# Kernel tuning notes

Hardware: AMD Instinct MI355X
Metric: run time of the kernel (lower is better)

Reference implementation:

```python
import jax, jax.numpy as jnp
import numpy as np

DIM = 256
N_CHANNELS = 8
NEIGHBORS = 16


def setup_inputs() -> dict:
    key = jax.random.key(0)
    kx, kw = jax.random.split(key)
    B, N, D = 4, 1024, DIM
    x = jax.random.normal(kx, (B, N, D), dtype=jnp.float32)
    # nn.Linear(dim, dim*2*n_channels, bias=False); store as [in, out] so y = x @ W
    W_qk = jax.random.normal(kw, (D, 2 * N_CHANNELS * D), dtype=jnp.float32) * (D ** -0.5)
    return {"x": x, "W_qk": W_qk}


def _norm_edge(edge):
    # edge: [B, C, N, N]
    norm_row = edge / (edge.sum(axis=-1, keepdims=True) + 1e-6)
    norm_col = norm_row / (norm_row.sum(axis=-2, keepdims=True) + 1e-6)
    # norm_row @ norm_col^T
    return jnp.einsum('bcnk,bcmk->bcnm', norm_row, norm_col)


def reference(x, W_qk):
    B, N, D = x.shape
    C = N_CHANNELS
    scale = D ** -0.5
    qk = (x @ W_qk).reshape(B, N, 2, C, D)
    q = jnp.transpose(qk[:, :, 0], (0, 2, 1, 3))  # [B, C, N, D]
    k = jnp.transpose(qk[:, :, 1], (0, 2, 1, 3))  # [B, C, N, D]
    attn = jax.nn.softmax(jnp.einsum('bcnd,bcmd->bcnm', q, k) * scale, axis=-1)

    # clip(): top-k neighbor mask from channel-summed (detached) attention
    sum_edge = jax.lax.stop_gradient(attn).sum(axis=1)  # [B, N, N]
    kk = min(NEIGHBORS, N)
    _, top_idx = jax.lax.top_k(sum_edge, kk)  # [B, N, kk]
    b_idx = jnp.arange(B)[:, None, None]
    r_idx = jnp.arange(N)[None, :, None]
    mask = jnp.zeros((B, N, N), dtype=attn.dtype).at[b_idx, r_idx, top_idx].set(1.0)
    mask = jnp.maximum(mask, jnp.eye(N, dtype=attn.dtype))  # identity diag
    edge = mask[:, None] * attn  # [B, C, N, N]
    return _norm_edge(edge)
```

## Files before the change

### kernel.cpp

```cpp
#include <hip/hip_runtime.h>
#include <hip/hip_bf16.h>
#include <math.h>

#define BB 4
#define NN 1024
#define DD 256
#define CC 8
#define KNBR 16
#define MAXSEL 17
#define ZCAP (NN * MAXSEL)

typedef _Float16 f16x8_t __attribute__((ext_vector_type(8)));
typedef _Float16 f16x4_t __attribute__((ext_vector_type(4)));
typedef float    f32x4_t __attribute__((ext_vector_type(4)));

__device__ __forceinline__ void gl2lds16(const _Float16* g, _Float16* ldsbase) {
    __builtin_amdgcn_global_load_lds(
        (const __attribute__((address_space(1))) unsigned int*)g,
        (__attribute__((address_space(3))) unsigned int*)ldsbase, 16, 0, 0);
}

__device__ __forceinline__ void split2(float v, _Float16& h, _Float16& l) {
    h = (_Float16)v;
    l = (_Float16)(v - (float)h);
}

__global__ __launch_bounds__(256) void split_all(const float* __restrict__ x,
                                                 const float* __restrict__ W,
                                                 _Float16* __restrict__ xh,
                                                 _Float16* __restrict__ xl,
                                                 _Float16* __restrict__ Wth,
                                                 _Float16* __restrict__ Wtl,
                                                 int* __restrict__ countb) {
    const int tid = threadIdx.x;
    if (blockIdx.x < 1024) {
        int i = (blockIdx.x * 256 + tid) * 4;
        float4 v = *(const float4*)(x + i);
        f16x4_t hv, lv;
        _Float16 h, l;
        split2(v.x, h, l); hv[0] = h; lv[0] = l;
        split2(v.y, h, l); hv[1] = h; lv[1] = l;
        split2(v.z, h, l); hv[2] = h; lv[2] = l;
        split2(v.w, h, l); hv[3] = h; lv[3] = l;
        *(f16x4_t*)(xh + i) = hv;
        *(f16x4_t*)(xl + i) = lv;
    } else {
        const int b2 = blockIdx.x - 1024;
        if (b2 == 0) {
            int4 zz = make_int4(0, 0, 0, 0);
#pragma unroll
            for (int g = 0; g < 4; g++) ((int4*)countb)[tid + 256 * g] = zz;
        }
        __shared__ float t[64][65];
        const int n0 = (b2 & 63) * 64;
        const int k0 = (b2 >> 6) * 64;
#pragma unroll
        for (int i = 0; i < 16; i++) {
            int k = i * 4 + (tid >> 6);
            int n = tid & 63;
            t[k][n] = W[(size_t)(k0 + k) * 4096 + n0 + n];
        }
        __syncthreads();
#pragma unroll
        for (int i = 0; i < 16; i++) {
            int n = i * 4 + (tid >> 6);
            int k = tid & 63;
            _Float16 h, l;
            split2(t[k][n] * 16.f, h, l);
            size_t o = (size_t)(n0 + n) * 256 + k0 + k;
            Wth[o] = h; Wtl[o] = l;
        }
    }
}

#define STG(dst, src, rowbase, kk)                                             \
    do {                                                                       \
        gl2lds16((src) + (size_t)((rowbase) + r_st) * 256 + (kk) + c8,         \
                 &(dst)[(w * 64) * 8]);                                        \
        gl2lds16((src) + (size_t)((rowbase) + 64 + r_st) * 256 + (kk) + c8,    \
                 &(dst)[(256 + w * 64) * 8]);                                  \
    } while (0)

#define MFMA3(accv, AH, AL, BH, BL)                                            \
    do {                                                                       \
        accv = __builtin_amdgcn_mfma_f32_16x16x32_f16(AL, BH, accv, 0, 0, 0);  \
        accv = __builtin_amdgcn_mfma_f32_16x16x32_f16(AH, BL, accv, 0, 0, 0);  \
        accv = __builtin_amdgcn_mfma_f32_16x16x32_f16(AH, BH, accv, 0, 0, 0);  \
    } while (0)

#define COMPUTE(AH, AL, BH, BL)                                                \
    do {                                                                       \
        f16x8_t ah[4], al[4];                                                  \
        _Pragma("unroll")                                                      \
        for (int mi = 0; mi < 4; mi++) {                                       \
            int r = (wr * 64 + mi * 16 + lm) * 32 + qx8;                       \
            ah[mi] = *(const f16x8_t*)&(AH)[r];                                \
            al[mi] = *(const f16x8_t*)&(AL)[r];                                \
        }                                                                      \
        _Pragma("unroll")                                                      \
        for (int ni = 0; ni < 4; ni++) {                                       \
            int rb = (wc * 64 + ni * 16 + lm) * 32 + qx8;                      \
            f16x8_t bh = *(const f16x8_t*)&(BH)[rb];                           \
            f16x8_t bl = *(const f16x8_t*)&(BL)[rb];                           \
            _Pragma("unroll")                                                  \
            for (int mi = 0; mi < 4; mi++)                                     \
                MFMA3(acc[mi][ni], ah[mi], al[mi], bh, bl);                    \
        }                                                                      \
    } while (0)

__global__ __launch_bounds__(256) void gemm_xw_mfma(
        const _Float16* __restrict__ xh, const _Float16* __restrict__ xl,
        const _Float16* __restrict__ wth, const _Float16* __restrict__ wtl,
        _Float16* __restrict__ qh, _Float16* __restrict__ ql,
        _Float16* __restrict__ kh, _Float16* __restrict__ kl) {
    __shared__ __align__(16) char smem[65536];
    _Float16* Ah0 = (_Float16*)smem;
    _Float16* Al0 = (_Float16*)(smem + 8192);
    _Float16* Bh0 = (_Float16*)(smem + 16384);
    _Float16* Bl0 = (_Float16*)(smem + 24576);
    _Float16* Ah1 = (_Float16*)(smem + 32768);
    _Float16* Al1 = (_Float16*)(smem + 40960);
    _Float16* Bh1 = (_Float16*)(smem + 49152);
    _Float16* Bl1 = (_Float16*)(smem + 57344);
    const int tid = threadIdx.x, lane = tid & 63, w = tid >> 6;
    const int wr = w >> 1, wc = w & 1;
    const int lm = lane & 15, quad = lane >> 4;
    const int row0 = blockIdx.y * 128, col0 = blockIdx.x * 128;
    const int r_st = tid >> 2;
    const int c8 = (((tid & 3) ^ ((tid >> 3) & 3)) * 8);
    const int qx8 = ((quad ^ ((lm >> 1) & 3)) * 8);

    f32x4_t acc[4][4];
#pragma unroll
    for (int i = 0; i < 4; i++)
#pragma unroll
        for (int j = 0; j < 4; j++) acc[i][j] = (f32x4_t)(0.f);

    STG(Ah0, xh, row0, 0); STG(Al0, xl, row0, 0);
    STG(Bh0, wth, col0, 0); STG(Bl0, wtl, col0, 0);
    __syncthreads();
#pragma unroll
    for (int t = 0; t < 8; t += 2) {
        {
            int kn = (t + 1) * 32;
            if (t + 1 < 8) {
                STG(Ah1, xh, row0, kn); STG(Al1, xl, row0, kn);
                STG(Bh1, wth, col0, kn); STG(Bl1, wtl, col0, kn);
            }
            COMPUTE(Ah0, Al0, Bh0, Bl0);
            __syncthreads();
        }
        {
            int kn = (t + 2) * 32;
            if (t + 2 < 8) {
                STG(Ah0, xh, row0, kn); STG(Al0, xl, row0, kn);
                STG(Bh0, wth, col0, kn); STG(Bl0, wtl, col0, kn);
            }
            COMPUTE(Ah1, Al1, Bh1, Bl1);
            __syncthreads();
        }
    }

    float* tr = (float*)smem;
    const int s = col0 >> 11, c = (col0 >> 8) & 7, dbase = col0 & 255;
    _Float16* dh = s ? kh : qh;
    _Float16* dl = s ? kl : ql;
    const int rl = tid >> 2;
    const int cb = (tid & 3) * 8;
#pragma unroll
    for (int p = 0; p < 2; p++) {
        if (p) __syncthreads();
        if (wr == p) {
#pragma unroll
            for (int mi = 0; mi < 4; mi++) {
                int rloc = mi * 16 + quad * 4;
#pragma unroll
                for (int ni = 0; ni < 4; ni++) {
                    int cl = wc * 64 + ni * 16 + lm;
#pragma unroll
                    for (int r = 0; r < 4; r++)
                        tr[(rloc + r) * 132 + cl] = acc[mi][ni][r];
                }
            }
        }
        __syncthreads();
        int rr = row0 + p * 64 + rl;
        int bb = rr >> 10, n = rr & 1023;
        size_t base = (((size_t)(bb * CC + c)) * NN + n) * DD + dbase;
#pragma unroll
        for (int g = 0; g < 4; g++) {
            int ccol = g * 32 + cb;
            f16x8_t hv, lv;
#pragma unroll
            for (int e = 0; e < 8; e++) {
                float vv = tr[rl * 132 + ccol + e];
                _Float16 h, l;
                split2(vv, h, l);
                hv[e] = h; lv[e] = l;
            }
            *(f16x8_t*)(dh + base + ccol) = hv;
            *(f16x8_t*)(dl + base + ccol) = lv;
        }
    }
}

__global__ __launch_bounds__(256) void gemm_qkt_mfma(
        const _Float16* __restrict__ qh, const _Float16* __restrict__ ql,
        const _Float16* __restrict__ kh, const _Float16* __restrict__ kl,
        float* __restrict__ attn) {
    __shared__ __align__(16) char smem[65536];
    _Float16* Ah0 = (_Float16*)smem;
    _Float16* Al0 = (_Float16*)(smem + 8192);
    _Float16* Bh0 = (_Float16*)(smem + 16384);
    _Float16* Bl0 = (_Float16*)(smem + 24576);
    _Float16* Ah1 = (_Float16*)(smem + 32768);
    _Float16* Al1 = (_Float16*)(smem + 40960);
    _Float16* Bh1 = (_Float16*)(smem + 49152);
    _Float16* Bl1 = (_Float16*)(smem + 57344);
    const int tid = threadIdx.x, lane = tid & 63, w = tid >> 6;
    const int wr = w >> 1, wc = w & 1;
    const int lm = lane & 15, quad = lane >> 4;
    const int id = blockIdx.x;
    const int rb8 = id & 7, qq = id >> 3;
    const int j = qq & 63, zhi = qq >> 6;
    const int z = zhi * 8 + rb8;
    const int row0 = (j >> 3) * 128, col0 = (j & 7) * 128;
    const size_t zo = (size_t)z * NN * DD;
    float* Cm = attn + (size_t)z * NN * NN;
    const int r_st = tid >> 2;
    const int c8 = (((tid & 3) ^ ((tid >> 3) & 3)) * 8);
    const int qx8 = ((quad ^ ((lm >> 1) & 3)) * 8);
    const float scale = 0.0625f / 256.0f;

    f32x4_t acc[4][4];
#pragma unroll
    for (int i = 0; i < 4; i++)
#pragma unroll
        for (int j2 = 0; j2 < 4; j2++) acc[i][j2] = (f32x4_t)(0.f);

    const _Float16* qhz = qh + zo;
    const _Float16* qlz = ql + zo;
    const _Float16* khz = kh + zo;
    const _Float16* klz = kl + zo;

    STG(Ah0, qhz, row0, 0); STG(Al0, qlz, row0, 0);
    STG(Bh0, khz, col0, 0); STG(Bl0, klz, col0, 0);
    __syncthreads();
#pragma unroll
    for (int t = 0; t < 8; t += 2) {
        {
            int kn = (t + 1) * 32;
            if (t + 1 < 8) {
                STG(Ah1, qhz, row0, kn); STG(Al1, qlz, row0, kn);
                STG(Bh1, khz, col0, kn); STG(Bl1, klz, col0, kn);
            }
            COMPUTE(Ah0, Al0, Bh0, Bl0);
            __syncthreads();
        }
        {
            int kn = (t + 2) * 32;
            if (t + 2 < 8) {
                STG(Ah0, qhz, row0, kn); STG(Al0, qlz, row0, kn);
                STG(Bh0, khz, col0, kn); STG(Bl0, klz, col0, kn);
            }
            COMPUTE(Ah1, Al1, Bh1, Bl1);
            __syncthreads();
        }
    }

#pragma unroll
    for (int mi = 0; mi < 4; mi++)
#pragma unroll
        for (int ni = 0; ni < 4; ni++) {
            int row = row0 + wr * 64 + mi * 16 + quad * 4;
            int col = col0 + wc * 64 + ni * 16 + lm;
#pragma unroll
            for (int r = 0; r < 4; r++)
                Cm[(size_t)(row + r) * NN + col] = acc[mi][ni][r] * scale;
        }
}

__global__ __launch_bounds__(256) void softmax_topk(const float* __restrict__ attn,
                                                    float2* __restrict__ ml,
                                                    int* __restrict__ idx,
                                                    int* __restrict__ cnt,
                                                    int* __restrict__ countb,
                                                    float* __restrict__ colsum) {
    __shared__ float psum[4][NN];
    __shared__ float cval[64];
    __shared__ int   cidx[64];
    __shared__ int fsel[MAXSEL];
    __shared__ int fcnt;
    const int bn = blockIdx.x, b = bn >> 10, n = bn & 1023;
    const int tid = threadIdx.x, lane = tid & 63, w = tid >> 6;

    if (tid < CC) colsum[(size_t)(b * CC + tid) * NN + n] = 0.f;

    const int colb = lane * 16;
    float4 u[2][4];
#pragma unroll
    for (int p = 0; p < 2; p++) {
        const int c = w * 2 + p;
        const float* rowp = attn + (((size_t)(b * CC + c) * NN + n) * NN) + colb;
#pragma unroll
        for (int g = 0; g < 4; g++) u[p][g] = *(const float4*)(rowp + g * 4);
    }

    float acc[16];
#pragma unroll
    for (int e = 0; e < 16; e++) acc[e] = 0.f;

#pragma unroll
    for (int p = 0; p < 2; p++) {
        const int c = w * 2 + p;
        const float* f = (const float*)&u[p][0];
        float mx = f[0];
#pragma unroll
        for (int e = 1; e < 16; e++) mx = fmaxf(mx, f[e]);
#pragma unroll
        for (int off = 1; off < 64; off <<= 1) mx = fmaxf(mx, __shfl_xor(mx, off));
        float sm = 0.f;
        float pe[16];
#pragma unroll
        for (int e = 0; e < 16; e++) { pe[e] = expf(f[e] - mx); sm += pe[e]; }
#pragma unroll
        for (int off = 1; off < 64; off <<= 1) sm += __shfl_xor(sm, off);
        if (lane == 0) ml[(size_t)(b * CC + c) * NN + n] = make_float2(mx, sm);
        float inv = 1.0f / sm;
#pragma unroll
        for (int e = 0; e < 16; e++) acc[e] += pe[e] * inv;
    }
#pragma unroll
    for (int g = 0; g < 4; g++)
        *(float4*)&psum[w][colb + g * 4] =
            make_float4(acc[g * 4], acc[g * 4 + 1], acc[g * 4 + 2], acc[g * 4 + 3]);
    __syncthreads();

    const int m4 = tid * 4;
    float4 a0 = *(const float4*)&psum[0][m4];
    float4 a1 = *(const float4*)&psum[1][m4];
    float4 a2 = *(const float4*)&psum[2][m4];
    float4 a3 = *(const float4*)&psum[3][m4];
    float v0 = a0.x + a1.x + a2.x + a3.x;
    float v1 = a0.y + a1.y + a2.y + a3.y;
    float v2 = a0.z + a1.z + a2.z + a3.z;
    float v3 = a0.w + a1.w + a2.w + a3.w;

    float myv = 0.f; int myi = 0;
    for (int it = 0; it < KNBR; it++) {
        float bv = v0; int bi = m4;
        if (v1 > bv) { bv = v1; bi = m4 + 1; }
        if (v2 > bv) { bv = v2; bi = m4 + 2; }
        if (v3 > bv) { bv = v3; bi = m4 + 3; }
#pragma unroll
        for (int off = 1; off < 64; off <<= 1) {
            float ov = __shfl_xor(bv, off);
            int oi = __shfl_xor(bi, off);
            if (ov > bv || (ov == bv && oi < bi)) { bv = ov; bi = oi; }
        }
        if (lane == it) { myv = bv; myi = bi; }
        v0 = (bi == m4)     ? -INFINITY : v0;
        v1 = (bi == m4 + 1) ? -INFINITY : v1;
        v2 = (bi == m4 + 2) ? -INFINITY : v2;
        v3 = (bi == m4 + 3) ? -INFINITY : v3;
    }
    if (lane < KNBR) { cval[w * KNBR + lane] = myv; cidx[w * KNBR + lane] = myi; }
    __syncthreads();

    if (w == 0) {
        float mv = cval[lane]; int mi = cidx[lane];
        for (int it = 0; it < KNBR; it++) {
            float bv = mv; int bi = mi;
#pragma unroll
            for (int off = 1; off < 64; off <<= 1) {
                float ov = __shfl_xor(bv, off);
                int oi = __shfl_xor(bi, off);
                if (ov > bv || (ov == bv && oi < bi)) { bv = ov; bi = oi; }
            }
            if (lane == 0) fsel[it] = bi;
            if (mi == bi) mv = -INFINITY;
        }
        if (lane == 0) {
            bool has = false;
            for (int t = 0; t < KNBR; t++)
                if (fsel[t] == n) has = true;
            int c = KNBR;
            if (!has) { fsel[KNBR] = n; c = KNBR + 1; }
            fcnt = c;
            cnt[bn] = c;
        }
    }
    __syncthreads();
    if (tid < fcnt) {
        idx[bn * MAXSEL + tid] = fsel[tid];
        atomicAdd(&countb[b * NN + fsel[tid]], 1);
    }
}

__global__ __launch_bounds__(256) void scan_offb(const int* __restrict__ countb,
                                                 int* __restrict__ offb,
                                                 int* __restrict__ curs) {
    __shared__ int wtot[4];
    const int b = blockIdx.x, tid = threadIdx.x, lane = tid & 63, w = tid >> 6;
    int c0 = countb[b * NN + tid * 4 + 0];
    int c1 = countb[b * NN + tid * 4 + 1];
    int c2 = countb[b * NN + tid * 4 + 2];
    int c3 = countb[b * NN + tid * 4 + 3];
    int tsum = c0 + c1 + c2 + c3;
    int incl = tsum;
#pragma unroll
    for (int off = 1; off < 64; off <<= 1) {
        int v = __shfl_up(incl, off);
        if (lane >= off) incl += v;
    }
    if (lane == 63) wtot[w] = incl;
    __syncthreads();
    int woff = 0;
    for (int i = 0; i < w; i++) woff += wtot[i];
    int base = woff + incl - tsum;
    int o0 = base, o1 = base + c0, o2 = base + c0 + c1, o3 = base + c0 + c1 + c2;
    offb[b * NN + tid * 4 + 0] = o0;
    offb[b * NN + tid * 4 + 1] = o1;
    offb[b * NN + tid * 4 + 2] = o2;
    offb[b * NN + tid * 4 + 3] = o3;
#pragma unroll
    for (int c = 0; c < CC; c++) {
        int z = b * CC + c;
        curs[z * NN + tid * 4 + 0] = o0;
        curs[z * NN + tid * 4 + 1] = o1;
        curs[z * NN + tid * 4 + 2] = o2;
        curs[z * NN + tid * 4 + 3] = o3;
    }
}

__global__ __launch_bounds__(256) void rownorm_fill(const float* __restrict__ attn,
                                                    const float2* __restrict__ ml,
                                                    const int* __restrict__ idx,
                                                    const int* __restrict__ cnt,
                                                    int* __restrict__ curs,
                                                    float* __restrict__ nr,
                                                    float* __restrict__ colsum,
                                                    int* __restrict__ eidx,
                                                    float* __restrict__ eval) {
    const int t = blockIdx.x * 256 + threadIdx.x;
    const int z = t >> 10, n = t & 1023;
    const int b = z >> 3;
    const int bn = b * NN + n;
    const int c_ = cnt[bn];
    const float* arow = attn + (size_t)t * NN;
    const float2 MM = ml[t];
    const float invl = 1.0f / MM.y;
    const size_t zb = (size_t)z * ZCAP;
    float a[MAXSEL];
    int kk[MAXSEL];
    float s = 0.f;
#pragma unroll
    for (int j = 0; j < MAXSEL; j++) {
        if (j < c_) {
            kk[j] = idx[bn * MAXSEL + j];
            float p = expf(arow[kk[j]] - MM.x) * invl;
            a[j] = p; s += p;
        }
    }
    const float inv = 1.f / (s + 1e-6f);
#pragma unroll
    for (int j = 0; j < MAXSEL; j++) {
        if (j < c_) {
            float v = a[j] * inv;
            nr[(size_t)t * MAXSEL + j] = v;
            atomicAdd(&colsum[(size_t)z * NN + kk[j]], v);
            int p = atomicAdd(&curs[z * NN + kk[j]], 1);
            eidx[zb + p] = n;
            eval[zb + p] = v;
        }
    }
}

__global__ __launch_bounds__(256) void out_sparse(const float* __restrict__ nr,
                                                  const int* __restrict__ idx,
                                                  const int* __restrict__ cnt,
                                                  const int* __restrict__ offb,
                                                  const int* __restrict__ countb,
                                                  const float* __restrict__ colsum,
                                                  const int* __restrict__ eidx,
                                                  const float* __restrict__ eval,
                                                  float* __restrict__ out) {
    __shared__ float row[NN];
    __shared__ float gscale[MAXSEL];
    __shared__ int goff[MAXSEL];
    __shared__ int glen[MAXSEL];
    const int t = blockIdx.x;
    const int z = t >> 10;
    const int b = z >> 3;
    const int bn = b * NN + (t & 1023);
    const int tid = threadIdx.x;
    const size_t zb = (size_t)z * ZCAP;

    ((float4*)row)[tid] = make_float4(0.f, 0.f, 0.f, 0.f);
    const int c_ = cnt[bn];
    if (tid < MAXSEL) {
        float sc = 0.f;
        int off = 0, len = 0;
        if (tid < c_) {
            int k = idx[bn * MAXSEL + tid];
            float wgt = nr[(size_t)t * MAXSEL + tid];
            sc = wgt / (colsum[(size_t)z * NN + k] + 1e-6f);
            off = offb[b * NN + k];
            len = countb[b * NN + k];
        }
        gscale[tid] = sc; goff[tid] = off; glen[tid] = len;
    }
    __syncthreads();
    const int j = tid / 15;
    const int lg = tid - j * 15;
    if (j < MAXSEL) {
        const float sc = gscale[j];
        const int off = goff[j], len = glen[j];
        for (int i = lg; i < len; i += 15) {
            int m = eidx[zb + off + i];
            float v = eval[zb + off + i];
            atomicAdd(&row[m], sc * v);
        }
    }
    __syncthreads();
    *(float4*)(out + (size_t)t * NN + tid * 4) = ((float4*)row)[tid];
}

extern "C" void kernel_launch(void* const* d_in, const int* in_sizes, int n_in,
                              void* d_out, int out_size, void* d_ws, size_t ws_size,
                              hipStream_t stream) {
    const float* x = (const float*)d_in[0];
    const float* W = (const float*)d_in[1];
    float* out = (float*)d_out;
    char* ws = (char*)d_ws;

    float* attn = (float*)d_out;

    _Float16* qh  = (_Float16*)(ws);
    _Float16* ql  = (_Float16*)(ws + 16777216ull);
    _Float16* kh  = (_Float16*)(ws + 33554432ull);
    _Float16* kl  = (_Float16*)(ws + 50331648ull);
    _Float16* xh  = (_Float16*)(ws + 67108864ull);
    _Float16* xl  = (_Float16*)(ws + 69206016ull);
    _Float16* wth = (_Float16*)(ws + 71303168ull);
    _Float16* wtl = (_Float16*)(ws + 73400320ull);
    int*    idx  = (int*)   (ws + 75497472ull);
    int*    cnt  = (int*)   (ws + 75776000ull);
    float*  nr   = (float*) (ws + 75792384ull);
    float*  colsum = (float*)(ws + 78020608ull);
    float2* ml   = (float2*)(ws + 78151680ull);
    int*    countb = (int*) (ws + 78413824ull);
    int*    offb = (int*)   (ws + 78430208ull);
    int*    curs = (int*)   (ws + 78446592ull);
    int*    eidx = (int*)   (ws + 78577664ull);
    float*  eval = (float*) (ws + 80805888ull);

    split_all<<<1280, 256, 0, stream>>>(x, W, xh, xl, wth, wtl, countb);
    gemm_xw_mfma<<<dim3(32, 32), 256, 0, stream>>>(xh, xl, wth, wtl,
                                                   qh, ql, kh, kl);
    gemm_qkt_mfma<<<2048, 256, 0, stream>>>(qh, ql, kh, kl, attn);
    softmax_topk<<<4096, 256, 0, stream>>>(attn, ml, idx, cnt, countb, colsum);
    scan_offb<<<4, 256, 0, stream>>>(countb, offb, curs);
    rownorm_fill<<<128, 256, 0, stream>>>(attn, ml, idx, cnt, curs, nr, colsum,
                                          eidx, eval);
    out_sparse<<<32768, 256, 0, stream>>>(nr, idx, cnt, offb, countb, colsum,
                                          eidx, eval, out);
}
```

Measured before the change: 411.8 us.

## Process one output row per wavefront with prefix-sum load balancing in out_sparse

The sparse output kernel now assigns one output row to each 64-lane wavefront (four rows per block) instead of one row per 256-thread block. A wavefront prefix scan over the selected neighbors' column lengths flattens the per-neighbor work, and each lane binary-searches that scan to find its entry, replacing the fixed 15-thread-per-neighbor split that left threads idle. Output rows are written with nontemporal stores. It needs more LDS per block and a per-entry binary search, but launches a quarter as many blocks with less imbalance.

```diff
diff --git a/kernel.cpp b/kernel.cpp
--- a/kernel.cpp
+++ b/kernel.cpp
@@ -485,45 +485,62 @@
                                                   const int* __restrict__ eidx,
                                                   const float* __restrict__ eval,
                                                   float* __restrict__ out) {
-    __shared__ float row[NN];
-    __shared__ float gscale[MAXSEL];
-    __shared__ int goff[MAXSEL];
-    __shared__ int glen[MAXSEL];
-    const int t = blockIdx.x;
+    __shared__ float row[4][NN];
+    __shared__ float gscale[4][MAXSEL];
+    __shared__ int   goff[4][MAXSEL];
+    __shared__ int   gpref[4][MAXSEL + 1];
+    const int tid = threadIdx.x, lane = tid & 63, w = tid >> 6;
+    const int t = blockIdx.x * 4 + w;
     const int z = t >> 10;
     const int b = z >> 3;
     const int bn = b * NN + (t & 1023);
-    const int tid = threadIdx.x;
     const size_t zb = (size_t)z * ZCAP;
 
-    ((float4*)row)[tid] = make_float4(0.f, 0.f, 0.f, 0.f);
+    f32x4_t zz = (f32x4_t)(0.f);
+#pragma unroll
+    for (int q = 0; q < 4; q++) ((f32x4_t*)row[w])[q * 64 + lane] = zz;
+
     const int c_ = cnt[bn];
-    if (tid < MAXSEL) {
-        float sc = 0.f;
-        int off = 0, len = 0;
-        if (tid < c_) {
-            int k = idx[bn * MAXSEL + tid];
-            float wgt = nr[(size_t)t * MAXSEL + tid];
-            sc = wgt / (colsum[(size_t)z * NN + k] + 1e-6f);
-            off = offb[b * NN + k];
-            len = countb[b * NN + k];
-        }
-        gscale[tid] = sc; goff[tid] = off; glen[tid] = len;
-    }
-    __syncthreads();
-    const int j = tid / 15;
-    const int lg = tid - j * 15;
-    if (j < MAXSEL) {
-        const float sc = gscale[j];
-        const int off = goff[j], len = glen[j];
-        for (int i = lg; i < len; i += 15) {
-            int m = eidx[zb + off + i];
-            float v = eval[zb + off + i];
-            atomicAdd(&row[m], sc * v);
-        }
-    }
-    __syncthreads();
-    *(float4*)(out + (size_t)t * NN + tid * 4) = ((float4*)row)[tid];
+    float sc = 0.f;
+    int off = 0, len = 0;
+    if (lane < c_) {
+        int k = idx[bn * MAXSEL + lane];
+        float wgt = nr[(size_t)t * MAXSEL + lane];
+        sc = wgt / (colsum[(size_t)z * NN + k] + 1e-6f);
+        off = offb[b * NN + k];
+        len = countb[b * NN + k];
+    }
+    int incl = len;
+#pragma unroll
+    for (int o = 1; o < 32; o <<= 1) {
+        int v = __shfl_up(incl, o);
+        if (lane >= o) incl += v;
+    }
+    if (lane < MAXSEL) { gscale[w][lane] = sc; goff[w][lane] = off; }
+    if (lane <= MAXSEL) gpref[w][lane] = incl - len;
+    __syncthreads();
+
+    const int tot = gpref[w][MAXSEL];
+    for (int e = lane; e < tot; e += 64) {
+        int lo = 0, hi = MAXSEL;
+        while (hi - lo > 1) {
+            int mid = (lo + hi) >> 1;
+            if (gpref[w][mid] <= e) lo = mid; else hi = mid;
+        }
+        int i = e - gpref[w][lo] + goff[w][lo];
+        int m = eidx[zb + i];
+        float v = eval[zb + i];
+        atomicAdd(&row[w][m], gscale[w][lo] * v);
+    }
+    __syncthreads();
+
+    const size_t ob = (size_t)t * NN;
+    f32x4_t* op = (f32x4_t*)(out + ob);
+#pragma unroll
+    for (int q = 0; q < 4; q++) {
+        f32x4_t vo = ((f32x4_t*)row[w])[q * 64 + lane];
+        __builtin_nontemporal_store(vo, op + q * 64 + lane);
+    }
 }
 
 extern "C" void kernel_launch(void* const* d_in, const int* in_sizes, int n_in,
@@ -563,6 +580,6 @@
     scan_offb<<<4, 256, 0, stream>>>(countb, offb, curs);
     rownorm_fill<<<128, 256, 0, stream>>>(attn, ml, idx, cnt, curs, nr, colsum,
                                           eidx, eval);
-    out_sparse<<<32768, 256, 0, stream>>>(nr, idx, cnt, offb, countb, colsum,
-                                          eidx, eval, out);
-}
+    out_sparse<<<8192, 256, 0, stream>>>(nr, idx, cnt, offb, countb, colsum,
+                                         eidx, eval, out);
+}
```

Result: slower. 421.3 us (+2.3%).
